# Kernel tuning notes

Measured on AMD Instinct MI355X. Metric: run time of the kernel, lower is better.

## Reference

```python
import jax, jax.numpy as jnp
import numpy as np

E, T, D, I, G, K = 8, 1024, 1024, 5632, 128, 2  # experts, tokens, hidden, intermediate, gptq group, topk
RENORMALIZE = True


def setup_inputs() -> dict:
    key = jax.random.key(0)
    ks = jax.random.split(key, 6)
    x = jax.random.normal(ks[0], (T, D), dtype=jnp.float32)
    gating_output = jax.random.normal(ks[1], (T, E), dtype=jnp.float32)
    # int4 GPTQ nibbles stored as int32 in [0, 16)
    w1_q = jax.random.randint(ks[2], (E, D, 2 * I), 0, 16, dtype=jnp.int32)
    w2_q = jax.random.randint(ks[3], (E, I, D), 0, 16, dtype=jnp.int32)
    # per-group scales (group size G along the input/contraction dim)
    w1_scale = jax.random.uniform(ks[4], (E, D // G, 2 * I), dtype=jnp.float32) * 0.02
    w2_scale = jax.random.uniform(ks[5], (E, I // G, D), dtype=jnp.float32) * 0.02
    return {"x": x, "gating_output": gating_output, "w1_q": w1_q, "w2_q": w2_q,
            "w1_scale": w1_scale, "w2_scale": w2_scale}


def _dequant(q, scale, group_size):
    # symmetric GPTQ int4: w = (q - 8) * scale, scale broadcast over its group
    s = jnp.repeat(scale, group_size, axis=1)  # [E, Kdim, N]
    return (q.astype(scale.dtype) - 8.0) * s


def reference(x, gating_output, w1_q, w2_q, w1_scale, w2_scale):
    w1 = _dequant(w1_q, w1_scale, G)  # [E, D, 2I]
    w2 = _dequant(w2_q, w2_scale, G)  # [E, I, D]

    # top-k softmax routing (use_grouped_topk=False path)
    probs = jax.nn.softmax(gating_output, axis=-1)        # [T, E]
    topk_w, topk_i = jax.lax.top_k(probs, K)              # [T, K]
    if RENORMALIZE:
        topk_w = topk_w / jnp.sum(topk_w, axis=-1, keepdims=True)
    # dense combine weights [T, E] (zero where expert not selected)
    cw = jnp.sum(jax.nn.one_hot(topk_i, E, dtype=x.dtype) * topk_w[..., None], axis=1)

    # expert MLPs: silu(x @ Wg) * (x @ Wu) @ Wd
    h = jnp.einsum('td,edn->etn', x, w1)                  # [E, T, 2I]
    gate, up = h[..., :I], h[..., I:]
    act = jax.nn.silu(gate) * up                          # [E, T, I]
    y = jnp.einsum('eti,eid->etd', act, w2)               # [E, T, D]

    out = jnp.einsum('te,etd->td', cw, y)                 # [T, D]
    return out
```

## Files before the change

kernel.cpp:

```cpp
#include <hip/hip_runtime.h>
#include <cstdint>
#include <cstddef>

#define E_ 8
#define T_ 1024
#define D_ 1024
#define I_ 5632
#define TWO_I_ 11264
#define NPAD_MAX 2176
#define NGRP_MAX 136

#define WS_ACTF_B 65536
#define WS_XGF_B  (65536 + 24510464)
#define WS_Y_B    WS_XGF_B
#define WS_CNT   0
#define WS_BASEP 8
#define WS_ESLOT 16
#define WS_TOKW  2064
#define WS_ETOK  4112

typedef __attribute__((ext_vector_type(8))) __bf16 bf16x8;
typedef __attribute__((ext_vector_type(4))) float  f32x4;

__device__ __forceinline__ unsigned f2bf(float f) {
    unsigned u = __float_as_uint(f);
    u += 0x7fffu + ((u >> 16) & 1u);
    return u >> 16;
}
__device__ __forceinline__ unsigned pack2bf(float f0, float f1) {
    unsigned a0 = __float_as_uint(f0); a0 += 0x7fffu + ((a0 >> 16) & 1u);
    unsigned a1 = __float_as_uint(f1); a1 += 0x7fffu + ((a1 >> 16) & 1u);
    return (a0 >> 16) | (a1 & 0xffff0000u);
}
#define QC(P, c) ((c) == 0 ? (P).x : (c) == 1 ? (P).y : (c) == 2 ? (P).z : (P).w)

__global__ void routing_kernel(const float* __restrict__ gate,
                               int* cnt, int* basep, int* eslot,
                               float* tokw, int* etok)
{
    int t = threadIdx.x;
    if (t < E_) cnt[t] = 0;
    __syncthreads();
    float g[E_];
#pragma unroll
    for (int e = 0; e < E_; ++e) g[e] = gate[t * E_ + e];
    int i0 = 0; float p0 = g[0];
#pragma unroll
    for (int e = 1; e < E_; ++e) if (g[e] > p0) { p0 = g[e]; i0 = e; }
    int i1 = -1; float p1 = -1e30f;
#pragma unroll
    for (int e = 0; e < E_; ++e) if (e != i0 && g[e] > p1) { p1 = g[e]; i1 = e; }
    float w0 = 1.0f / (1.0f + expf(p1 - p0));
    float w1 = 1.0f - w0;
    int s0 = atomicAdd(&cnt[i0], 1);
    int s1 = atomicAdd(&cnt[i1], 1);
    etok[i0 * T_ + s0] = t;
    etok[i1 * T_ + s1] = t;
    eslot[t * 2 + 0] = i0 * T_ + s0;  tokw[t * 2 + 0] = w0;
    eslot[t * 2 + 1] = i1 * T_ + s1;  tokw[t * 2 + 1] = w1;
    __syncthreads();
    if (t == 0) {
        int r = 0;
#pragma unroll
        for (int e = 0; e < E_; ++e) { basep[e] = r; r += (cnt[e] + 15) & ~15; }
    }
}

__global__ void gather_cast_kernel(const float* __restrict__ x,
                                   const int* __restrict__ cnt,
                                   const int* __restrict__ basep,
                                   const int* __restrict__ etok,
                                   unsigned short* __restrict__ xgf)
{
    int e = blockIdx.x >> 6, g = blockIdx.x & 63;
    int n = cnt[e];
    if (g * 16 >= n) return;
    int tid = threadIdx.x;
    int row = g * 16 + (tid & 15);
    row = min(row, n - 1);
    int tok = etok[e * T_ + row];
    const float* xr = x + (size_t)tok * D_;
    unsigned short* dst = xgf + ((size_t)(basep[e] >> 4) + g) * 16384;
#pragma unroll
    for (int it = 0; it < 8; ++it) {
        int c = it * 16 + (tid >> 4);
        float4 v0 = *(const float4*)(xr + c * 8);
        float4 v1 = *(const float4*)(xr + c * 8 + 4);
        uint4 h;
        h.x = pack2bf(v0.x, v0.y); h.y = pack2bf(v0.z, v0.w);
        h.z = pack2bf(v1.x, v1.y); h.w = pack2bf(v1.z, v1.w);
        *(uint4*)(dst + c * 128 + (tid & 15) * 8) = h;
    }
}

__global__ __launch_bounds__(256, 3) void gemm1_kernel(
    const unsigned short* __restrict__ xgf, const int* __restrict__ w1q,
    const float* __restrict__ w1s, const int* __restrict__ cnt,
    const int* __restrict__ basep, unsigned short* __restrict__ actf)
{
    __shared__ unsigned char blds[2][16384];
    int b = blockIdx.x;
    int xcd = b & 7, sl = b >> 3;
    int q5 = sl / 5, rb = sl - q5 * 5;
    int cb = q5 * 8 + xcd;
    int e = cb / 88, cg = cb - e * 88;

    int n = cnt[e];
    if (n <= 0) return;
    int npad = (n + 15) & ~15;
    if (rb * 64 >= npad) return;
    int pb = basep[e];

    int tid = threadIdx.x, lane = tid & 63, w = tid >> 6;
    int l15 = lane & 15, lq = lane >> 4;

    int colq = tid & 31, kc = tid >> 5;
    int bcol = colq * 4;
    int jb = (bcol < 64) ? (cg * 64 + bcol) : (I_ + cg * 64 + (bcol - 64));
    const int*   gq  = w1q + ((size_t)e * 1024 + kc * 8) * TWO_I_ + jb;
    const float* sqp = w1s + (size_t)e * 8 * TWO_I_ + jb;
    int fcw  = colq >> 2;
    int pzw  = (fcw & 3) | ((fcw >> 2) << 4);
    int lanp = (kc & 3) * 16 + (colq & 3) * 4;
    unsigned wbase = (unsigned)fcw * 2048 + (unsigned)(kc >> 2) * 1024;
    unsigned wro[4];
#pragma unroll
    for (int c = 0; c < 4; ++c)
        wro[c] = wbase + (unsigned)(((lanp + c) ^ pzw) << 4);

    unsigned rg0 = (unsigned)w * 2048 + (unsigned)((lane ^ w) << 4);
    int pzu = w | 16;
    unsigned ru0 = (unsigned)(w + 4) * 2048 + (unsigned)((lane ^ pzu) << 4);

    const char* abase = (const char*)xgf + lane * 16;

    int4 P[8]; float4 SS;

#define G1_ISSUE(S)                                                         \
    { _Pragma("unroll")                                                     \
      for (int j_ = 0; j_ < 8; ++j_)                                        \
          P[j_] = *(const int4*)(gq + (size_t)((S) * 64 + j_) * TWO_I_);    \
      SS = *(const float4*)(sqp + (size_t)((S) >> 1) * TWO_I_); }

#define G1_DEQW(S)                                                          \
    { unsigned char* bp_ = &blds[(S) & 1][0];                               \
      _Pragma("unroll")                                                     \
      for (int c_ = 0; c_ < 4; ++c_) {                                      \
          float s_ = QC(SS, c_); float o_ = -8.f * s_;                      \
          uint4 h_;                                                         \
          h_.x = pack2bf((float)QC(P[0], c_) * s_ + o_, (float)QC(P[1], c_) * s_ + o_); \
          h_.y = pack2bf((float)QC(P[2], c_) * s_ + o_, (float)QC(P[3], c_) * s_ + o_); \
          h_.z = pack2bf((float)QC(P[4], c_) * s_ + o_, (float)QC(P[5], c_) * s_ + o_); \
          h_.w = pack2bf((float)QC(P[6], c_) * s_ + o_, (float)QC(P[7], c_) * s_ + o_); \
          *(uint4*)(bp_ + wro[c_]) = h_;                                    \
      } }

    for (int tb = rb * 64; tb < npad; tb += 320) {
        int aoff[4];
#pragma unroll
        for (int mi = 0; mi < 4; ++mi) {
            int R = tb + mi * 16;
            R = min(R, npad - 16);
            aoff[mi] = ((pb + R) >> 4) * 32768;
        }
        f32x4 accg[4], accu[4];
#pragma unroll
        for (int mi = 0; mi < 4; ++mi) {
            accg[mi] = (f32x4){0.f, 0.f, 0.f, 0.f};
            accu[mi] = (f32x4){0.f, 0.f, 0.f, 0.f};
        }

        G1_ISSUE(0)
        G1_DEQW(0)
        asm volatile("s_waitcnt lgkmcnt(0)" ::: "memory");
        __builtin_amdgcn_s_barrier();
        asm volatile("" ::: "memory");

#pragma unroll 2
        for (int st = 0; st < 16; ++st) {
            const char* at = abase + (size_t)st * 2048;
            bf16x8 a0[4], a1[4];
#pragma unroll
            for (int mi = 0; mi < 4; ++mi)
                a0[mi] = *(const bf16x8*)(at + aoff[mi]);
#pragma unroll
            for (int mi = 0; mi < 4; ++mi)
                a1[mi] = *(const bf16x8*)(at + 1024 + aoff[mi]);
            if (st + 1 < 16) { G1_ISSUE(st + 1) }
            const unsigned char* bp = &blds[st & 1][0];
            bf16x8 bg0 = *(const bf16x8*)(bp + rg0);
            bf16x8 bu0 = *(const bf16x8*)(bp + ru0);
            bf16x8 bg1 = *(const bf16x8*)(bp + rg0 + 1024);
            bf16x8 bu1 = *(const bf16x8*)(bp + ru0 + 1024);
            __builtin_amdgcn_s_setprio(1);
#pragma unroll
            for (int mi = 0; mi < 4; ++mi) {
                accg[mi] = __builtin_amdgcn_mfma_f32_16x16x32_bf16(a0[mi], bg0, accg[mi], 0, 0, 0);
                accu[mi] = __builtin_amdgcn_mfma_f32_16x16x32_bf16(a0[mi], bu0, accu[mi], 0, 0, 0);
            }
#pragma unroll
            for (int mi = 0; mi < 4; ++mi) {
                accg[mi] = __builtin_amdgcn_mfma_f32_16x16x32_bf16(a1[mi], bg1, accg[mi], 0, 0, 0);
                accu[mi] = __builtin_amdgcn_mfma_f32_16x16x32_bf16(a1[mi], bu1, accu[mi], 0, 0, 0);
            }
            __builtin_amdgcn_s_setprio(0);
            if (st + 1 < 16) { G1_DEQW(st + 1) }
            asm volatile("s_waitcnt lgkmcnt(0)" ::: "memory");
            __builtin_amdgcn_s_barrier();
            asm volatile("" ::: "memory");
        }

#pragma unroll
        for (int mi = 0; mi < 4; ++mi) {
#pragma unroll
            for (int r = 0; r < 4; ++r) {
                int m = tb + mi * 16 + lq * 4 + r;
                if (m < npad) {
                    float gv = accg[mi][r], uv = accu[mi][r];
                    float av = gv / (1.f + __expf(-gv)) * uv;
                    int prow = pb + m;
                    int icol = cg * 64 + w * 16 + l15;
                    size_t o = (size_t)(prow >> 4) * 90112 + (icol >> 3) * 128
                             + (prow & 15) * 8 + (icol & 7);
                    actf[o] = (unsigned short)f2bf(av);
                }
            }
        }
    }
#undef G1_ISSUE
#undef G1_DEQW
}

__global__ __launch_bounds__(256, 3) void gemm2_kernel(
    const unsigned short* __restrict__ actf, const int* __restrict__ w2q,
    const float* __restrict__ w2s, const int* __restrict__ cnt,
    const int* __restrict__ basep, float* __restrict__ y)
{
    __shared__ unsigned char blds[2][16384];
    int b = blockIdx.x;
    int xcd = b & 7, sl = b >> 3;
    int q5 = sl / 5, rb = sl - q5 * 5;
    int cb = q5 * 8 + xcd;
    int e = cb >> 5, r5 = cb & 31;
    int dt = r5 >> 2, seg = r5 & 3;

    int n = cnt[e];
    if (n <= 0) return;
    int npad = (n + 15) & ~15;
    if (rb * 64 >= npad) return;
    int pb = basep[e];

    int tid = threadIdx.x, lane = tid & 63, w = tid >> 6;
    int l15 = lane & 15, lq = lane >> 4;

    int colq = tid & 31, kc = tid >> 5;
    int colb = dt * 128 + colq * 4;
    const int*   gq  = w2q + ((size_t)e * 5632 + seg * 1408 + kc * 8) * 1024 + colb;
    const float* sqp = w2s + ((size_t)e * 44 + seg * 11) * 1024 + colb;
    int fcw  = colq >> 2;
    int pzw  = (fcw & 3) | ((fcw >> 2) << 4);
    int lanp = (kc & 3) * 16 + (colq & 3) * 4;
    unsigned wbase = (unsigned)fcw * 2048 + (unsigned)(kc >> 2) * 1024;
    unsigned wro[4];
#pragma unroll
    for (int c = 0; c < 4; ++c)
        wro[c] = wbase + (unsigned)(((lanp + c) ^ pzw) << 4);

    unsigned rg0 = (unsigned)w * 2048 + (unsigned)((lane ^ w) << 4);
    int pzu = w | 16;
    unsigned ru0 = (unsigned)(w + 4) * 2048 + (unsigned)((lane ^ pzu) << 4);

    const char* abase = (const char*)actf + seg * 45056 + lane * 16;

    int4 P[8]; float4 SS;

#define G2_ISSUE(S)                                                         \
    { _Pragma("unroll")                                                     \
      for (int j_ = 0; j_ < 8; ++j_)                                        \
          P[j_] = *(const int4*)(gq + (size_t)((S) * 64 + j_) * 1024);      \
      SS = *(const float4*)(sqp + (size_t)((S) >> 1) * 1024); }

#define G2_DEQW(S)                                                          \
    { unsigned char* bp_ = &blds[(S) & 1][0];                               \
      _Pragma("unroll")                                                     \
      for (int c_ = 0; c_ < 4; ++c_) {                                      \
          float s_ = QC(SS, c_); float o_ = -8.f * s_;                      \
          uint4 h_;                                                         \
          h_.x = pack2bf((float)QC(P[0], c_) * s_ + o_, (float)QC(P[1], c_) * s_ + o_); \
          h_.y = pack2bf((float)QC(P[2], c_) * s_ + o_, (float)QC(P[3], c_) * s_ + o_); \
          h_.z = pack2bf((float)QC(P[4], c_) * s_ + o_, (float)QC(P[5], c_) * s_ + o_); \
          h_.w = pack2bf((float)QC(P[6], c_) * s_ + o_, (float)QC(P[7], c_) * s_ + o_); \
          *(uint4*)(bp_ + wro[c_]) = h_;                                    \
      } }

    for (int tb = rb * 64; tb < npad; tb += 320) {
        int aoff[4];
#pragma unroll
        for (int mi = 0; mi < 4; ++mi) {
            int R = tb + mi * 16;
            R = min(R, npad - 16);
            aoff[mi] = ((pb + R) >> 4) * 180224;
        }
        f32x4 acc0[4], acc1[4];
#pragma unroll
        for (int mi = 0; mi < 4; ++mi) {
            acc0[mi] = (f32x4){0.f, 0.f, 0.f, 0.f};
            acc1[mi] = (f32x4){0.f, 0.f, 0.f, 0.f};
        }

        G2_ISSUE(0)
        G2_DEQW(0)
        asm volatile("s_waitcnt lgkmcnt(0)" ::: "memory");
        __builtin_amdgcn_s_barrier();
        asm volatile("" ::: "memory");

#pragma unroll 2
        for (int st = 0; st < 22; ++st) {
            const char* at = abase + (size_t)st * 2048;
            bf16x8 a0[4], a1[4];
#pragma unroll
            for (int mi = 0; mi < 4; ++mi)
                a0[mi] = *(const bf16x8*)(at + aoff[mi]);
#pragma unroll
            for (int mi = 0; mi < 4; ++mi)
                a1[mi] = *(const bf16x8*)(at + 1024 + aoff[mi]);
            if (st + 1 < 22) { G2_ISSUE(st + 1) }
            const unsigned char* bp = &blds[st & 1][0];
            bf16x8 b00 = *(const bf16x8*)(bp + rg0);
            bf16x8 b10 = *(const bf16x8*)(bp + ru0);
            bf16x8 b01 = *(const bf16x8*)(bp + rg0 + 1024);
            bf16x8 b11 = *(const bf16x8*)(bp + ru0 + 1024);
            __builtin_amdgcn_s_setprio(1);
#pragma unroll
            for (int mi = 0; mi < 4; ++mi) {
                acc0[mi] = __builtin_amdgcn_mfma_f32_16x16x32_bf16(a0[mi], b00, acc0[mi], 0, 0, 0);
                acc1[mi] = __builtin_amdgcn_mfma_f32_16x16x32_bf16(a0[mi], b10, acc1[mi], 0, 0, 0);
            }
#pragma unroll
            for (int mi = 0; mi < 4; ++mi) {
                acc0[mi] = __builtin_amdgcn_mfma_f32_16x16x32_bf16(a1[mi], b01, acc0[mi], 0, 0, 0);
                acc1[mi] = __builtin_amdgcn_mfma_f32_16x16x32_bf16(a1[mi], b11, acc1[mi], 0, 0, 0);
            }
            __builtin_amdgcn_s_setprio(0);
            if (st + 1 < 22) { G2_DEQW(st + 1) }
            asm volatile("s_waitcnt lgkmcnt(0)" ::: "memory");
            __builtin_amdgcn_s_barrier();
            asm volatile("" ::: "memory");
        }

#pragma unroll
        for (int mi = 0; mi < 4; ++mi) {
#pragma unroll
            for (int r = 0; r < 4; ++r) {
                int m = tb + mi * 16 + lq * 4 + r;
                if (m < n) {
                    float* yr = y + ((size_t)seg * NPAD_MAX + pb + m) * 1024;
                    int dc = dt * 128 + w * 16 + l15;
                    yr[dc]      = acc0[mi][r];
                    yr[dc + 64] = acc1[mi][r];
                }
            }
        }
    }
#undef G2_ISSUE
#undef G2_DEQW
}

__global__ void combine_kernel(const float* __restrict__ y,
                               const int* __restrict__ eslot,
                               const float* __restrict__ tokw,
                               const int* __restrict__ basep,
                               float* __restrict__ out)
{
    int idx = blockIdx.x * blockDim.x + threadIdx.x;
    int t  = idx >> 8;
    int dc = idx & 255;
    int es0 = eslot[t * 2 + 0], es1 = eslot[t * 2 + 1];
    float w0 = tokw[t * 2 + 0], w1 = tokw[t * 2 + 1];
    int p0 = basep[es0 >> 10] + (es0 & 1023);
    int p1 = basep[es1 >> 10] + (es1 & 1023);
    const float4* y4 = (const float4*)y;
    float4 o = (float4){0.f, 0.f, 0.f, 0.f};
#pragma unroll
    for (int seg = 0; seg < 4; ++seg) {
        float4 a = y4[((size_t)seg * NPAD_MAX + p0) * 256 + dc];
        float4 b = y4[((size_t)seg * NPAD_MAX + p1) * 256 + dc];
        o.x += w0 * a.x + w1 * b.x;
        o.y += w0 * a.y + w1 * b.y;
        o.z += w0 * a.z + w1 * b.z;
        o.w += w0 * a.w + w1 * b.w;
    }
    ((float4*)out)[idx] = o;
}

extern "C" void kernel_launch(void* const* d_in, const int* in_sizes, int n_in,
                              void* d_out, int out_size, void* d_ws, size_t ws_size,
                              hipStream_t stream)
{
    const float* x    = (const float*)d_in[0];
    const float* gate = (const float*)d_in[1];
    const int*   w1q  = (const int*)d_in[2];
    const int*   w2q  = (const int*)d_in[3];
    const float* w1s  = (const float*)d_in[4];
    const float* w2s  = (const float*)d_in[5];
    float* out = (float*)d_out;
    int*   wsi = (int*)d_ws;
    float* wsf = (float*)d_ws;

    int*   cnt   = wsi + WS_CNT;
    int*   basep = wsi + WS_BASEP;
    int*   eslot = wsi + WS_ESLOT;
    float* tokw  = wsf + WS_TOKW;
    int*   etok  = wsi + WS_ETOK;
    unsigned short* actf = (unsigned short*)((char*)d_ws + WS_ACTF_B);
    unsigned short* xgf  = (unsigned short*)((char*)d_ws + WS_XGF_B);
    float*          y    = (float*)((char*)d_ws + WS_Y_B);

    routing_kernel<<<1, 1024, 0, stream>>>(gate, cnt, basep, eslot, tokw, etok);
    gather_cast_kernel<<<E_ * 64, 256, 0, stream>>>(x, cnt, basep, etok, xgf);
    gemm1_kernel<<<E_ * 88 * 5, 256, 0, stream>>>(xgf, w1q, w1s, cnt, basep, actf);
    gemm2_kernel<<<E_ * 8 * 4 * 5, 256, 0, stream>>>(actf, w2q, w2s, cnt, basep, y);
    combine_kernel<<<(T_ * D_ / 4) / 256, 256, 0, stream>>>(y, eslot, tokw, basep, out);
}
```

Before: 817.6 us.

## Repack int4 weights to int8 per call and prefetch two stages ahead

```diff
diff --git a/kernel.cpp b/kernel.cpp
--- a/kernel.cpp
+++ b/kernel.cpp
@@ -13,6 +13,8 @@
 #define WS_ACTF_B 65536
 #define WS_XGF_B  (65536 + 24510464)
 #define WS_Y_B    WS_XGF_B
+#define WS_PB1_B  67108864
+#define WS_PB2_B  167772160
 #define WS_CNT   0
 #define WS_BASEP 8
 #define WS_ESLOT 16
@@ -93,17 +95,72 @@
     }
 }
 
+__global__ __launch_bounds__(256) void repack1_kernel(
+    const int* __restrict__ w1q, char* __restrict__ pb1)
+{
+    int b = blockIdx.x;
+    int cb = b % 11;  int t2 = b / 11;
+    int dc = t2 & 127; int e = t2 >> 7;
+    int tid = threadIdx.x;
+    int col = cb * 1024 + tid * 4;
+    const int* src = w1q + ((size_t)e * 1024 + dc * 8) * TWO_I_ + col;
+    uint4 q[8];
+#pragma unroll
+    for (int j = 0; j < 8; ++j)
+        q[j] = *(const uint4*)(src + (size_t)j * TWO_I_);
+    unsigned wo[8];
+#pragma unroll
+    for (int c = 0; c < 4; ++c) {
+#pragma unroll
+        for (int h = 0; h < 2; ++h) {
+            wo[c * 2 + h] = ((QC(q[4*h+0], c) - 8u) & 255u)
+                          | (((QC(q[4*h+1], c) - 8u) & 255u) << 8)
+                          | (((QC(q[4*h+2], c) - 8u) & 255u) << 16)
+                          | ((QC(q[4*h+3], c) - 8u) << 24);
+        }
+    }
+    char* dst = pb1 + ((size_t)(e * 128 + dc) * TWO_I_ + col) * 8;
+    *(uint4*)dst        = (uint4){wo[0], wo[1], wo[2], wo[3]};
+    *(uint4*)(dst + 16) = (uint4){wo[4], wo[5], wo[6], wo[7]};
+}
+
+__global__ __launch_bounds__(256) void repack2_kernel(
+    const int* __restrict__ w2q, char* __restrict__ pb2)
+{
+    int b = blockIdx.x;
+    int ic = b % 704; int e = b / 704;
+    int tid = threadIdx.x;
+    int col = tid * 4;
+    const int* src = w2q + ((size_t)e * 5632 + ic * 8) * 1024 + col;
+    uint4 q[8];
+#pragma unroll
+    for (int j = 0; j < 8; ++j)
+        q[j] = *(const uint4*)(src + (size_t)j * 1024);
+    unsigned wo[8];
+#pragma unroll
+    for (int c = 0; c < 4; ++c) {
+#pragma unroll
+        for (int h = 0; h < 2; ++h) {
+            wo[c * 2 + h] = ((QC(q[4*h+0], c) - 8u) & 255u)
+                          | (((QC(q[4*h+1], c) - 8u) & 255u) << 8)
+                          | (((QC(q[4*h+2], c) - 8u) & 255u) << 16)
+                          | ((QC(q[4*h+3], c) - 8u) << 24);
+        }
+    }
+    char* dst = pb2 + ((size_t)(e * 704 + ic) * 1024 + col) * 8;
+    *(uint4*)dst        = (uint4){wo[0], wo[1], wo[2], wo[3]};
+    *(uint4*)(dst + 16) = (uint4){wo[4], wo[5], wo[6], wo[7]};
+}
+
 __global__ __launch_bounds__(256, 3) void gemm1_kernel(
-    const unsigned short* __restrict__ xgf, const int* __restrict__ w1q,
+    const unsigned short* __restrict__ xgf, const char* __restrict__ pb1,
     const float* __restrict__ w1s, const int* __restrict__ cnt,
     const int* __restrict__ basep, unsigned short* __restrict__ actf)
 {
     __shared__ unsigned char blds[2][16384];
     int b = blockIdx.x;
-    int xcd = b & 7, sl = b >> 3;
-    int q5 = sl / 5, rb = sl - q5 * 5;
-    int cb = q5 * 8 + xcd;
-    int e = cb / 88, cg = cb - e * 88;
+    int rb = b % 5; int t2 = b / 5;
+    int cg = t2 % 88; int e = t2 / 88;
 
     int n = cnt[e];
     if (n <= 0) return;
@@ -114,45 +171,50 @@
     int tid = threadIdx.x, lane = tid & 63, w = tid >> 6;
     int l15 = lane & 15, lq = lane >> 4;
 
-    int colq = tid & 31, kc = tid >> 5;
-    int bcol = colq * 4;
-    int jb = (bcol < 64) ? (cg * 64 + bcol) : (I_ + cg * 64 + (bcol - 64));
-    const int*   gq  = w1q + ((size_t)e * 1024 + kc * 8) * TWO_I_ + jb;
-    const float* sqp = w1s + (size_t)e * 8 * TWO_I_ + jb;
-    int fcw  = colq >> 2;
-    int pzw  = (fcw & 3) | ((fcw >> 2) << 4);
-    int lanp = (kc & 3) * 16 + (colq & 3) * 4;
-    unsigned wbase = (unsigned)fcw * 2048 + (unsigned)(kc >> 2) * 1024;
-    unsigned wro[4];
+    int colq = tid & 127, kh = tid >> 7;
+    int jb = (colq < 64) ? (cg * 64 + colq) : (I_ + cg * 64 + (colq - 64));
+    const char*  bq = pb1 + ((size_t)e * 128 * TWO_I_ + jb) * 8;
+    const float* sq = w1s + (size_t)e * 8 * TWO_I_ + jb;
+    int fcw = colq >> 4;
+    int pzw = (fcw & 3) | ((fcw >> 2) << 4);
+    unsigned wcell[4];
 #pragma unroll
     for (int c = 0; c < 4; ++c)
-        wro[c] = wbase + (unsigned)(((lanp + c) ^ pzw) << 4);
+        wcell[c] = (unsigned)fcw * 2048 + (unsigned)kh * 1024
+                 + (unsigned)(((c * 16 + (colq & 15)) ^ pzw) << 4);
 
     unsigned rg0 = (unsigned)w * 2048 + (unsigned)((lane ^ w) << 4);
-    int pzu = w | 16;
-    unsigned ru0 = (unsigned)(w + 4) * 2048 + (unsigned)((lane ^ pzu) << 4);
+    unsigned ru0 = (unsigned)(w + 4) * 2048 + (unsigned)((lane ^ (w | 16)) << 4);
 
     const char* abase = (const char*)xgf + lane * 16;
 
-    int4 P[8]; float4 SS;
-
-#define G1_ISSUE(S)                                                         \
+    uint2 Pa[4], Pb[4]; float Sa, Sb;
+
+#define G1_ISSUE(S, P, SS)                                                  \
     { _Pragma("unroll")                                                     \
-      for (int j_ = 0; j_ < 8; ++j_)                                        \
-          P[j_] = *(const int4*)(gq + (size_t)((S) * 64 + j_) * TWO_I_);    \
-      SS = *(const float4*)(sqp + (size_t)((S) >> 1) * TWO_I_); }
-
-#define G1_DEQW(S)                                                          \
+      for (int c_ = 0; c_ < 4; ++c_)                                        \
+          P[c_] = *(const uint2*)(bq + (size_t)((S) * 8 + kh * 4 + c_) * 90112); \
+      SS = sq[(size_t)((S) >> 1) * TWO_I_]; }
+
+#define G1_DEQW(S, P, SS)                                                   \
     { unsigned char* bp_ = &blds[(S) & 1][0];                               \
       _Pragma("unroll")                                                     \
       for (int c_ = 0; c_ < 4; ++c_) {                                      \
-          float s_ = QC(SS, c_); float o_ = -8.f * s_;                      \
+          unsigned px_ = P[c_].x, py_ = P[c_].y;                            \
+          float f0_ = (float)(int)(char)(px_);                              \
+          float f1_ = (float)(int)(char)(px_ >> 8);                         \
+          float f2_ = (float)(int)(char)(px_ >> 16);                        \
+          float f3_ = (float)((int)px_ >> 24);                              \
+          float f4_ = (float)(int)(char)(py_);                              \
+          float f5_ = (float)(int)(char)(py_ >> 8);                         \
+          float f6_ = (float)(int)(char)(py_ >> 16);                        \
+          float f7_ = (float)((int)py_ >> 24);                              \
           uint4 h_;                                                         \
-          h_.x = pack2bf((float)QC(P[0], c_) * s_ + o_, (float)QC(P[1], c_) * s_ + o_); \
-          h_.y = pack2bf((float)QC(P[2], c_) * s_ + o_, (float)QC(P[3], c_) * s_ + o_); \
-          h_.z = pack2bf((float)QC(P[4], c_) * s_ + o_, (float)QC(P[5], c_) * s_ + o_); \
-          h_.w = pack2bf((float)QC(P[6], c_) * s_ + o_, (float)QC(P[7], c_) * s_ + o_); \
-          *(uint4*)(bp_ + wro[c_]) = h_;                                    \
+          h_.x = pack2bf(f0_ * SS, f1_ * SS);                               \
+          h_.y = pack2bf(f2_ * SS, f3_ * SS);                               \
+          h_.z = pack2bf(f4_ * SS, f5_ * SS);                               \
+          h_.w = pack2bf(f6_ * SS, f7_ * SS);                               \
+          *(uint4*)(bp_ + wcell[c_]) = h_;                                  \
       } }
 
     for (int tb = rb * 64; tb < npad; tb += 320) {
@@ -170,8 +232,9 @@
             accu[mi] = (f32x4){0.f, 0.f, 0.f, 0.f};
         }
 
-        G1_ISSUE(0)
-        G1_DEQW(0)
+        G1_ISSUE(0, Pa, Sa)
+        G1_ISSUE(1, Pb, Sb)
+        G1_DEQW(0, Pa, Sa)
         asm volatile("s_waitcnt lgkmcnt(0)" ::: "memory");
         __builtin_amdgcn_s_barrier();
         asm volatile("" ::: "memory");
@@ -186,7 +249,10 @@
 #pragma unroll
             for (int mi = 0; mi < 4; ++mi)
                 a1[mi] = *(const bf16x8*)(at + 1024 + aoff[mi]);
-            if (st + 1 < 16) { G1_ISSUE(st + 1) }
+            if (st + 2 < 16) {
+                if (st & 1) { G1_ISSUE(st + 2, Pb, Sb) }
+                else        { G1_ISSUE(st + 2, Pa, Sa) }
+            }
             const unsigned char* bp = &blds[st & 1][0];
             bf16x8 bg0 = *(const bf16x8*)(bp + rg0);
             bf16x8 bu0 = *(const bf16x8*)(bp + ru0);
@@ -204,7 +270,10 @@
                 accu[mi] = __builtin_amdgcn_mfma_f32_16x16x32_bf16(a1[mi], bu1, accu[mi], 0, 0, 0);
             }
             __builtin_amdgcn_s_setprio(0);
-            if (st + 1 < 16) { G1_DEQW(st + 1) }
+            if (st + 1 < 16) {
+                if (st & 1) { G1_DEQW(st + 1, Pa, Sa) }
+                else        { G1_DEQW(st + 1, Pb, Sb) }
+            }
             asm volatile("s_waitcnt lgkmcnt(0)" ::: "memory");
             __builtin_amdgcn_s_barrier();
             asm volatile("" ::: "memory");
@@ -232,17 +301,14 @@
 }
 
 __global__ __launch_bounds__(256, 3) void gemm2_kernel(
-    const unsigned short* __restrict__ actf, const int* __restrict__ w2q,
+    const unsigned short* __restrict__ actf, const char* __restrict__ pb2,
     const float* __restrict__ w2s, const int* __restrict__ cnt,
     const int* __restrict__ basep, float* __restrict__ y)
 {
     __shared__ unsigned char blds[2][16384];
     int b = blockIdx.x;
-    int xcd = b & 7, sl = b >> 3;
-    int q5 = sl / 5, rb = sl - q5 * 5;
-    int cb = q5 * 8 + xcd;
-    int e = cb >> 5, r5 = cb & 31;
-    int dt = r5 >> 2, seg = r5 & 3;
+    int rb = b % 5; int t2 = b / 5;
+    int seg = t2 & 3, dt = (t2 >> 2) & 7, e = t2 >> 5;
 
     int n = cnt[e];
     if (n <= 0) return;
@@ -253,44 +319,50 @@
     int tid = threadIdx.x, lane = tid & 63, w = tid >> 6;
     int l15 = lane & 15, lq = lane >> 4;
 
-    int colq = tid & 31, kc = tid >> 5;
-    int colb = dt * 128 + colq * 4;
-    const int*   gq  = w2q + ((size_t)e * 5632 + seg * 1408 + kc * 8) * 1024 + colb;
-    const float* sqp = w2s + ((size_t)e * 44 + seg * 11) * 1024 + colb;
-    int fcw  = colq >> 2;
-    int pzw  = (fcw & 3) | ((fcw >> 2) << 4);
-    int lanp = (kc & 3) * 16 + (colq & 3) * 4;
-    unsigned wbase = (unsigned)fcw * 2048 + (unsigned)(kc >> 2) * 1024;
-    unsigned wro[4];
+    int colq = tid & 127, kh = tid >> 7;
+    int dcol = dt * 128 + colq;
+    const char*  bq = pb2 + ((size_t)(e * 704 + seg * 176) * 1024 + dcol) * 8;
+    const float* sq = w2s + ((size_t)e * 44 + seg * 11) * 1024 + dcol;
+    int fcw = colq >> 4;
+    int pzw = (fcw & 3) | ((fcw >> 2) << 4);
+    unsigned wcell[4];
 #pragma unroll
     for (int c = 0; c < 4; ++c)
-        wro[c] = wbase + (unsigned)(((lanp + c) ^ pzw) << 4);
+        wcell[c] = (unsigned)fcw * 2048 + (unsigned)kh * 1024
+                 + (unsigned)(((c * 16 + (colq & 15)) ^ pzw) << 4);
 
     unsigned rg0 = (unsigned)w * 2048 + (unsigned)((lane ^ w) << 4);
-    int pzu = w | 16;
-    unsigned ru0 = (unsigned)(w + 4) * 2048 + (unsigned)((lane ^ pzu) << 4);
+    unsigned ru0 = (unsigned)(w + 4) * 2048 + (unsigned)((lane ^ (w | 16)) << 4);
 
     const char* abase = (const char*)actf + seg * 45056 + lane * 16;
 
-    int4 P[8]; float4 SS;
-
-#define G2_ISSUE(S)                                                         \
+    uint2 Pa[4], Pb[4]; float Sa, Sb;
+
+#define G2_ISSUE(S, P, SS)                                                  \
     { _Pragma("unroll")                                                     \
-      for (int j_ = 0; j_ < 8; ++j_)                                        \
-          P[j_] = *(const int4*)(gq + (size_t)((S) * 64 + j_) * 1024);      \
-      SS = *(const float4*)(sqp + (size_t)((S) >> 1) * 1024); }
-
-#define G2_DEQW(S)                                                          \
+      for (int c_ = 0; c_ < 4; ++c_)                                        \
+          P[c_] = *(const uint2*)(bq + (size_t)((S) * 8 + kh * 4 + c_) * 8192); \
+      SS = sq[(size_t)((S) >> 1) * 1024]; }
+
+#define G2_DEQW(S, P, SS)                                                   \
     { unsigned char* bp_ = &blds[(S) & 1][0];                               \
       _Pragma("unroll")                                                     \
       for (int c_ = 0; c_ < 4; ++c_) {                                      \
-          float s_ = QC(SS, c_); float o_ = -8.f * s_;                      \
+          unsigned px_ = P[c_].x, py_ = P[c_].y;                            \
+          float f0_ = (float)(int)(char)(px_);                              \
+          float f1_ = (float)(int)(char)(px_ >> 8);                         \
+          float f2_ = (float)(int)(char)(px_ >> 16);                        \
+          float f3_ = (float)((int)px_ >> 24);                              \
+          float f4_ = (float)(int)(char)(py_);                              \
+          float f5_ = (float)(int)(char)(py_ >> 8);                         \
+          float f6_ = (float)(int)(char)(py_ >> 16);                        \
+          float f7_ = (float)((int)py_ >> 24);                              \
           uint4 h_;                                                         \
-          h_.x = pack2bf((float)QC(P[0], c_) * s_ + o_, (float)QC(P[1], c_) * s_ + o_); \
-          h_.y = pack2bf((float)QC(P[2], c_) * s_ + o_, (float)QC(P[3], c_) * s_ + o_); \
-          h_.z = pack2bf((float)QC(P[4], c_) * s_ + o_, (float)QC(P[5], c_) * s_ + o_); \
-          h_.w = pack2bf((float)QC(P[6], c_) * s_ + o_, (float)QC(P[7], c_) * s_ + o_); \
-          *(uint4*)(bp_ + wro[c_]) = h_;                                    \
+          h_.x = pack2bf(f0_ * SS, f1_ * SS);                               \
+          h_.y = pack2bf(f2_ * SS, f3_ * SS);                               \
+          h_.z = pack2bf(f4_ * SS, f5_ * SS);                               \
+          h_.w = pack2bf(f6_ * SS, f7_ * SS);                               \
+          *(uint4*)(bp_ + wcell[c_]) = h_;                                  \
       } }
 
     for (int tb = rb * 64; tb < npad; tb += 320) {
@@ -308,8 +380,9 @@
             acc1[mi] = (f32x4){0.f, 0.f, 0.f, 0.f};
         }
 
-        G2_ISSUE(0)
-        G2_DEQW(0)
+        G2_ISSUE(0, Pa, Sa)
+        G2_ISSUE(1, Pb, Sb)
+        G2_DEQW(0, Pa, Sa)
         asm volatile("s_waitcnt lgkmcnt(0)" ::: "memory");
         __builtin_amdgcn_s_barrier();
         asm volatile("" ::: "memory");
@@ -324,7 +397,10 @@
 #pragma unroll
             for (int mi = 0; mi < 4; ++mi)
                 a1[mi] = *(const bf16x8*)(at + 1024 + aoff[mi]);
-            if (st + 1 < 22) { G2_ISSUE(st + 1) }
+            if (st + 2 < 22) {
+                if (st & 1) { G2_ISSUE(st + 2, Pb, Sb) }
+                else        { G2_ISSUE(st + 2, Pa, Sa) }
+            }
             const unsigned char* bp = &blds[st & 1][0];
             bf16x8 b00 = *(const bf16x8*)(bp + rg0);
             bf16x8 b10 = *(const bf16x8*)(bp + ru0);
@@ -342,7 +418,10 @@
                 acc1[mi] = __builtin_amdgcn_mfma_f32_16x16x32_bf16(a1[mi], b11, acc1[mi], 0, 0, 0);
             }
             __builtin_amdgcn_s_setprio(0);
-            if (st + 1 < 22) { G2_DEQW(st + 1) }
+            if (st + 1 < 22) {
+                if (st & 1) { G2_DEQW(st + 1, Pa, Sa) }
+                else        { G2_DEQW(st + 1, Pb, Sb) }
+            }
             asm volatile("s_waitcnt lgkmcnt(0)" ::: "memory");
             __builtin_amdgcn_s_barrier();
             asm volatile("" ::: "memory");
@@ -415,10 +494,14 @@
     unsigned short* actf = (unsigned short*)((char*)d_ws + WS_ACTF_B);
     unsigned short* xgf  = (unsigned short*)((char*)d_ws + WS_XGF_B);
     float*          y    = (float*)((char*)d_ws + WS_Y_B);
+    char*           pb1  = (char*)d_ws + WS_PB1_B;
+    char*           pb2  = (char*)d_ws + WS_PB2_B;
 
     routing_kernel<<<1, 1024, 0, stream>>>(gate, cnt, basep, eslot, tokw, etok);
     gather_cast_kernel<<<E_ * 64, 256, 0, stream>>>(x, cnt, basep, etok, xgf);
-    gemm1_kernel<<<E_ * 88 * 5, 256, 0, stream>>>(xgf, w1q, w1s, cnt, basep, actf);
-    gemm2_kernel<<<E_ * 8 * 4 * 5, 256, 0, stream>>>(actf, w2q, w2s, cnt, basep, y);
+    repack1_kernel<<<E_ * 128 * 11, 256, 0, stream>>>(w1q, pb1);
+    repack2_kernel<<<E_ * 704, 256, 0, stream>>>(w2q, pb2);
+    gemm1_kernel<<<E_ * 88 * 5, 256, 0, stream>>>(xgf, pb1, w1s, cnt, basep, actf);
+    gemm2_kernel<<<E_ * 8 * 4 * 5, 256, 0, stream>>>(actf, pb2, w2s, cnt, basep, y);
     combine_kernel<<<(T_ * D_ / 4) / 256, 256, 0, stream>>>(y, eslot, tokw, basep, out);
 }
```

After: 832.6 us. About the same (+1.8%).
